# Optimization experiments

Hardware: AMD Instinct MI355X
Metric: run time of the kernel (lower is better)

## Reference

```python
import jax, jax.numpy as jnp
import numpy as np

IN_DIM = 512
OUT_DIM = 512
DEGREE = 3
KNOTS = (0.2, 0.4, 0.6, 0.8)
SDIM = DEGREE + 1 + len(KNOTS)  # 8
BATCH = 2048


def truncated_power_basis(t):
    # t: (B,) -> (B, SDIM)
    cols = [jnp.ones_like(t)]
    for p in range(1, DEGREE + 1):
        cols.append(t ** p)
    for c in KNOTS:  # degree > 1 branch: relu(t - knot)^degree
        cols.append(jax.nn.relu(t - c) ** DEGREE)
    return jnp.stack(cols, axis=1)


def setup_inputs() -> dict:
    key = jax.random.key(0)
    k0, k1, k2 = jax.random.split(key, 3)
    inputs = jax.random.uniform(k0, (BATCH, IN_DIM + 1), dtype=jnp.float32)
    # xavier_uniform for W_wts (fan_in=SDIM, fan_out=IN_DIM*OUT_DIM)
    limW = float(np.sqrt(6.0 / (SDIM + IN_DIM * OUT_DIM)))
    W_wts = jax.random.uniform(k1, (SDIM, IN_DIM * OUT_DIM), dtype=jnp.float32,
                               minval=-limW, maxval=limW)
    limb = float(np.sqrt(6.0 / (SDIM + OUT_DIM)))
    b_wts = jax.random.uniform(k2, (SDIM, OUT_DIM), dtype=jnp.float32,
                               minval=-limb, maxval=limb)
    return {"inputs": inputs, "W_wts": W_wts, "b_wts": b_wts}


def reference(inputs, W_wts, b_wts):
    treatment = inputs[:, 0]          # (B,)
    features = inputs[:, 1:]          # (B, IN_DIM)
    basis = truncated_power_basis(treatment)  # (B, SDIM)
    Wk = W_wts.reshape(SDIM, IN_DIM, OUT_DIM)
    # fused: per-sample weight W[b] = sum_s basis[b,s] * Wk[s]; out[b] = features[b] @ W[b]
    out = jnp.einsum('bs,bi,sio->bo', basis, features, Wk)
    out = out + basis @ b_wts         # (B, OUT_DIM)
    return out
```

## Files before the change

kernel.cpp:

```cpp
#include <hip/hip_runtime.h>
#include <stdint.h>

#define BATCH   2048
#define INDIM   512
#define OUTDIM  512
#define KP      4352
#define NBLK_A  2048
#define NBLK_B  544
#define SPLITK  4
#define KSTEPS  17

typedef __attribute__((ext_vector_type(4))) float  f32x4;
typedef __attribute__((ext_vector_type(8))) __bf16 bf16x8;
typedef __attribute__((ext_vector_type(8))) unsigned short u16x8;
typedef __attribute__((ext_vector_type(4))) unsigned short u16x4;

__device__ __forceinline__ unsigned short f2bf(float x) {
  unsigned int u = __float_as_uint(x);
  u += 0x7fffu + ((u >> 16) & 1u);
  return (unsigned short)(u >> 16);
}

__device__ __forceinline__ void llds16(const void* g, void* s) {
  __builtin_amdgcn_global_load_lds(
      (__attribute__((address_space(1))) void*)g,
      (__attribute__((address_space(3))) void*)s, 16, 0, 0);
}

__global__ __launch_bounds__(256) void prep_kernel(
    const float* __restrict__ inp, const float* __restrict__ W,
    const float* __restrict__ bwts, unsigned short* __restrict__ Abf,
    unsigned short* __restrict__ Btf) {
  const int tid = threadIdx.x;
  const int bx  = blockIdx.x;
  if (bx < NBLK_A) {
    const float* row = inp + (size_t)bx * (INDIM + 1);
    const float t = row[0];
    float bs[8];
    bs[0] = 1.0f; bs[1] = t; bs[2] = t * t; bs[3] = bs[2] * t;
    const float kn[4] = {0.2f, 0.4f, 0.6f, 0.8f};
#pragma unroll
    for (int c = 0; c < 4; ++c) {
      float d = fmaxf(t - kn[c], 0.0f);
      bs[4 + c] = d * d * d;
    }
    unsigned short* Arow = Abf + (size_t)bx * KP;
    for (int k4 = tid * 4; k4 < KP; k4 += 1024) {
      float v0, v1, v2, v3;
      if (k4 < 4096) {
        const float s = bs[k4 >> 9];
        const int i = k4 & 511;
        v0 = s * row[1 + i]; v1 = s * row[2 + i];
        v2 = s * row[3 + i]; v3 = s * row[4 + i];
      } else if (k4 < 4104) {
        const int s0 = k4 - 4096;
        v0 = bs[s0]; v1 = bs[s0 + 1]; v2 = bs[s0 + 2]; v3 = bs[s0 + 3];
      } else {
        v0 = v1 = v2 = v3 = 0.0f;
      }
      u16x4 o;
      o.x = f2bf(v0); o.y = f2bf(v1); o.z = f2bf(v2); o.w = f2bf(v3);
      *(u16x4*)&Arow[k4] = o;
    }
  } else {
    const int bb = bx - NBLK_A;
    const int kt = bb >> 3, ntile = bb & 7;
    const int k0 = kt * 64, n0 = ntile * 64;
    __shared__ float Ts[64][65];
#pragma unroll
    for (int p = 0; p < 4; ++p) {
      const int r  = (tid >> 4) + p * 16;
      const int c4 = (tid & 15) * 4;
      const int k  = k0 + r;
      float4 v;
      if (k < 4096)      v = *(const float4*)&W[(size_t)k * 512 + n0 + c4];
      else if (k < 4104) v = *(const float4*)&bwts[(size_t)(k - 4096) * 512 + n0 + c4];
      else               v = make_float4(0.f, 0.f, 0.f, 0.f);
      Ts[c4 + 0][r] = v.x; Ts[c4 + 1][r] = v.y;
      Ts[c4 + 2][r] = v.z; Ts[c4 + 3][r] = v.w;
    }
    __syncthreads();
    const int nl  = tid >> 2;
    const int kcc = (tid & 3) * 16;
    u16x8 o0, o1;
#pragma unroll
    for (int q = 0; q < 8; ++q) {
      o0[q] = f2bf(Ts[nl][kcc + q]);
      o1[q] = f2bf(Ts[nl][kcc + 8 + q]);
    }
    unsigned short* dst = Btf + (size_t)(n0 + nl) * KP + k0 + kcc;
    *(u16x8*)dst = o0;
    *(u16x8*)(dst + 8) = o1;
  }
}

__global__ __launch_bounds__(256, 4) void gemm_kernel(
    const unsigned short* __restrict__ Abf,
    const unsigned short* __restrict__ Btf,
    float* __restrict__ out) {
  const int tid  = threadIdx.x;
  const int kc   = blockIdx.x & (SPLITK - 1);
  const int tile = blockIdx.x >> 2;
  const int nt = tile & 7, mt = tile >> 3;
  const int m0 = mt * 64, n0 = nt * 64;
  const int l = tid & 63, w = tid >> 6;
  const int wm = w >> 1, wn = w & 1;
  const int quad = l >> 4, lr = l & 15;

  __shared__ __align__(16) unsigned short As[64 * 64];
  __shared__ __align__(16) unsigned short Bs[64 * 64];

  f32x4 acc00 = {}, acc01 = {}, acc10 = {}, acc11 = {};

  const int sr = tid >> 3, pc = tid & 7;
  const int lc = pc ^ (sr & 7);
  const unsigned short* Ag = Abf + (size_t)(m0 + sr) * KP + lc * 8;
  const unsigned short* Bg = Btf + (size_t)(n0 + sr) * KP + lc * 8;
  unsigned short* AsW = &As[sr * 64 + pc * 8];
  unsigned short* BsW = &Bs[sr * 64 + pc * 8];

  const int sx  = lr & 7;
  const int ar  = (wm * 32 + lr) * 64;
  const int br  = (wn * 32 + lr) * 64;
  const int c0  = ((0 + quad) ^ sx) * 8;
  const int c1  = ((4 + quad) ^ sx) * 8;

  int koff = kc * (KSTEPS * 64);
  for (int it = 0; it < KSTEPS; ++it) {
    llds16(Ag + koff,           AsW);
    llds16(Ag + koff + 32 * KP, AsW + 32 * 64);
    llds16(Bg + koff,           BsW);
    llds16(Bg + koff + 32 * KP, BsW + 32 * 64);
    __syncthreads();

    bf16x8 a00 = *(const bf16x8*)&As[ar + c0];
    bf16x8 a10 = *(const bf16x8*)&As[ar + 1024 + c0];
    bf16x8 b00 = *(const bf16x8*)&Bs[br + c0];
    bf16x8 b10 = *(const bf16x8*)&Bs[br + 1024 + c0];
    bf16x8 a01 = *(const bf16x8*)&As[ar + c1];
    bf16x8 a11 = *(const bf16x8*)&As[ar + 1024 + c1];
    bf16x8 b01 = *(const bf16x8*)&Bs[br + c1];
    bf16x8 b11 = *(const bf16x8*)&Bs[br + 1024 + c1];

    acc00 = __builtin_amdgcn_mfma_f32_16x16x32_bf16(a00, b00, acc00, 0, 0, 0);
    acc01 = __builtin_amdgcn_mfma_f32_16x16x32_bf16(a00, b10, acc01, 0, 0, 0);
    acc10 = __builtin_amdgcn_mfma_f32_16x16x32_bf16(a10, b00, acc10, 0, 0, 0);
    acc11 = __builtin_amdgcn_mfma_f32_16x16x32_bf16(a10, b10, acc11, 0, 0, 0);
    acc00 = __builtin_amdgcn_mfma_f32_16x16x32_bf16(a01, b01, acc00, 0, 0, 0);
    acc01 = __builtin_amdgcn_mfma_f32_16x16x32_bf16(a01, b11, acc01, 0, 0, 0);
    acc10 = __builtin_amdgcn_mfma_f32_16x16x32_bf16(a11, b01, acc10, 0, 0, 0);
    acc11 = __builtin_amdgcn_mfma_f32_16x16x32_bf16(a11, b11, acc11, 0, 0, 0);

    __syncthreads();
    koff += 64;
  }

  const int col = n0 + wn * 32 + lr;
  const int row = m0 + wm * 32 + quad * 4;
  float* o00 = out + (size_t)row * OUTDIM + col;
#pragma unroll
  for (int r = 0; r < 4; ++r) {
    unsafeAtomicAdd(o00 + (size_t)r * OUTDIM,             acc00[r]);
    unsafeAtomicAdd(o00 + (size_t)r * OUTDIM + 16,        acc01[r]);
    unsafeAtomicAdd(o00 + (size_t)(16 + r) * OUTDIM,      acc10[r]);
    unsafeAtomicAdd(o00 + (size_t)(16 + r) * OUTDIM + 16, acc11[r]);
  }
}

extern "C" void kernel_launch(void* const* d_in, const int* in_sizes, int n_in,
                              void* d_out, int out_size, void* d_ws, size_t ws_size,
                              hipStream_t stream) {
  const float* inp  = (const float*)d_in[0];
  const float* W    = (const float*)d_in[1];
  const float* bwts = (const float*)d_in[2];
  float* out = (float*)d_out;

  unsigned short* Abf = (unsigned short*)d_ws;
  unsigned short* Btf = Abf + (size_t)BATCH * KP;

  hipMemsetAsync(d_out, 0, (size_t)BATCH * OUTDIM * sizeof(float), stream);
  prep_kernel<<<NBLK_A + NBLK_B, 256, 0, stream>>>(inp, W, bwts, Abf, Btf);
  gemm_kernel<<<(BATCH / 64) * (OUTDIM / 64) * SPLITK, 256, 0, stream>>>(Abf, Btf, out);
}
```

Measured before the change: 101.9 us.

## Factor basis scaling out of GEMM: per-slice feature GEMM then scale by basis

The 2048x4352 basis-scaled activation matrix is no longer materialised. The GEMM now loads the bf16 features (2048x512) directly, computes a partial product for each basis slice, and scales it in fp32 by that row's basis value. The bias term basis@b_wts is computed in the prep kernel and written straight to the output, which removes the memset. This cuts prep-kernel write traffic and lets the A tile come from a much smaller, cache-resident array, at the cost of some extra fp32 FMAs per slice.

```diff
diff --git a/kernel.cpp b/kernel.cpp
--- a/kernel.cpp
+++ b/kernel.cpp
@@ -4,16 +4,13 @@
 #define BATCH   2048
 #define INDIM   512
 #define OUTDIM  512
-#define KP      4352
-#define NBLK_A  2048
-#define NBLK_B  544
+#define SDIM    8
+#define KTOT    4096
 #define SPLITK  4
-#define KSTEPS  17
 
 typedef __attribute__((ext_vector_type(4))) float  f32x4;
 typedef __attribute__((ext_vector_type(8))) __bf16 bf16x8;
 typedef __attribute__((ext_vector_type(8))) unsigned short u16x8;
-typedef __attribute__((ext_vector_type(4))) unsigned short u16x4;
 
 __device__ __forceinline__ unsigned short f2bf(float x) {
   unsigned int u = __float_as_uint(x);
@@ -27,55 +24,32 @@
       (__attribute__((address_space(3))) void*)s, 16, 0, 0);
 }
 
+__device__ __forceinline__ void mkbasis(float t, float* bs) {
+  bs[0] = 1.0f; bs[1] = t; bs[2] = t * t; bs[3] = bs[2] * t;
+  const float kn[4] = {0.2f, 0.4f, 0.6f, 0.8f};
+#pragma unroll
+  for (int c = 0; c < 4; ++c) {
+    float d = fmaxf(t - kn[c], 0.0f);
+    bs[4 + c] = d * d * d;
+  }
+}
+
 __global__ __launch_bounds__(256) void prep_kernel(
     const float* __restrict__ inp, const float* __restrict__ W,
-    const float* __restrict__ bwts, unsigned short* __restrict__ Abf,
-    unsigned short* __restrict__ Btf) {
+    const float* __restrict__ bwts, unsigned short* __restrict__ Fbf,
+    unsigned short* __restrict__ Btf, float* __restrict__ Bas,
+    float* __restrict__ out) {
   const int tid = threadIdx.x;
   const int bx  = blockIdx.x;
-  if (bx < NBLK_A) {
-    const float* row = inp + (size_t)bx * (INDIM + 1);
-    const float t = row[0];
-    float bs[8];
-    bs[0] = 1.0f; bs[1] = t; bs[2] = t * t; bs[3] = bs[2] * t;
-    const float kn[4] = {0.2f, 0.4f, 0.6f, 0.8f};
-#pragma unroll
-    for (int c = 0; c < 4; ++c) {
-      float d = fmaxf(t - kn[c], 0.0f);
-      bs[4 + c] = d * d * d;
-    }
-    unsigned short* Arow = Abf + (size_t)bx * KP;
-    for (int k4 = tid * 4; k4 < KP; k4 += 1024) {
-      float v0, v1, v2, v3;
-      if (k4 < 4096) {
-        const float s = bs[k4 >> 9];
-        const int i = k4 & 511;
-        v0 = s * row[1 + i]; v1 = s * row[2 + i];
-        v2 = s * row[3 + i]; v3 = s * row[4 + i];
-      } else if (k4 < 4104) {
-        const int s0 = k4 - 4096;
-        v0 = bs[s0]; v1 = bs[s0 + 1]; v2 = bs[s0 + 2]; v3 = bs[s0 + 3];
-      } else {
-        v0 = v1 = v2 = v3 = 0.0f;
-      }
-      u16x4 o;
-      o.x = f2bf(v0); o.y = f2bf(v1); o.z = f2bf(v2); o.w = f2bf(v3);
-      *(u16x4*)&Arow[k4] = o;
-    }
-  } else {
-    const int bb = bx - NBLK_A;
-    const int kt = bb >> 3, ntile = bb & 7;
+  if (bx < 512) {
+    const int kt = bx >> 3, ntile = bx & 7;
     const int k0 = kt * 64, n0 = ntile * 64;
     __shared__ float Ts[64][65];
 #pragma unroll
     for (int p = 0; p < 4; ++p) {
       const int r  = (tid >> 4) + p * 16;
       const int c4 = (tid & 15) * 4;
-      const int k  = k0 + r;
-      float4 v;
-      if (k < 4096)      v = *(const float4*)&W[(size_t)k * 512 + n0 + c4];
-      else if (k < 4104) v = *(const float4*)&bwts[(size_t)(k - 4096) * 512 + n0 + c4];
-      else               v = make_float4(0.f, 0.f, 0.f, 0.f);
+      float4 v = *(const float4*)&W[(size_t)(k0 + r) * 512 + n0 + c4];
       Ts[c4 + 0][r] = v.x; Ts[c4 + 1][r] = v.y;
       Ts[c4 + 2][r] = v.z; Ts[c4 + 3][r] = v.w;
     }
@@ -88,15 +62,47 @@
       o0[q] = f2bf(Ts[nl][kcc + q]);
       o1[q] = f2bf(Ts[nl][kcc + 8 + q]);
     }
-    unsigned short* dst = Btf + (size_t)(n0 + nl) * KP + k0 + kcc;
+    unsigned short* dst = Btf + (size_t)(n0 + nl) * KTOT + k0 + kcc;
     *(u16x8*)dst = o0;
     *(u16x8*)(dst + 8) = o1;
+  } else if (bx < 1024) {
+    const int b0   = (bx - 512) * 4;
+    const int b    = b0 + (tid >> 6);
+    const int i0   = (tid & 63) * 8;
+    const float* row = inp + (size_t)b * (INDIM + 1);
+    u16x8 o;
+#pragma unroll
+    for (int q = 0; q < 8; ++q) o[q] = f2bf(row[1 + i0 + q]);
+    *(u16x8*)(Fbf + (size_t)b * INDIM + i0) = o;
+    if (tid < 4) {
+      const int bb = b0 + tid;
+      float t = inp[(size_t)bb * (INDIM + 1)];
+      float bs[8]; mkbasis(t, bs);
+      f32x4 lo = {bs[0], bs[1], bs[2], bs[3]};
+      f32x4 hi = {bs[4], bs[5], bs[6], bs[7]};
+      *(f32x4*)(Bas + (size_t)bb * 8)     = lo;
+      *(f32x4*)(Bas + (size_t)bb * 8 + 4) = hi;
+    }
+  } else {
+    const int bb = (bx - 1024) * 2 + (tid >> 7);
+    const int o0 = (tid & 127) * 4;
+    float t = inp[(size_t)bb * (INDIM + 1)];
+    float bs[8]; mkbasis(t, bs);
+    float4 a = make_float4(0.f, 0.f, 0.f, 0.f);
+#pragma unroll
+    for (int s = 0; s < 8; ++s) {
+      float4 wv = *(const float4*)&bwts[s * OUTDIM + o0];
+      a.x += bs[s] * wv.x; a.y += bs[s] * wv.y;
+      a.z += bs[s] * wv.z; a.w += bs[s] * wv.w;
+    }
+    *(float4*)&out[(size_t)bb * OUTDIM + o0] = a;
   }
 }
 
 __global__ __launch_bounds__(256, 4) void gemm_kernel(
-    const unsigned short* __restrict__ Abf,
+    const unsigned short* __restrict__ Fbf,
     const unsigned short* __restrict__ Btf,
+    const float* __restrict__ Bas,
     float* __restrict__ out) {
   const int tid  = threadIdx.x;
   const int kc   = blockIdx.x & (SPLITK - 1);
@@ -110,12 +116,12 @@
   __shared__ __align__(16) unsigned short As[64 * 64];
   __shared__ __align__(16) unsigned short Bs[64 * 64];
 
-  f32x4 acc00 = {}, acc01 = {}, acc10 = {}, acc11 = {};
+  f32x4 m00 = {}, m01 = {}, m10 = {}, m11 = {};
 
   const int sr = tid >> 3, pc = tid & 7;
   const int lc = pc ^ (sr & 7);
-  const unsigned short* Ag = Abf + (size_t)(m0 + sr) * KP + lc * 8;
-  const unsigned short* Bg = Btf + (size_t)(n0 + sr) * KP + lc * 8;
+  const unsigned short* Ag = Fbf + (size_t)(m0 + sr) * INDIM + lc * 8;
+  const unsigned short* Bg = Btf + (size_t)(n0 + sr) * KTOT + lc * 8;
   unsigned short* AsW = &As[sr * 64 + pc * 8];
   unsigned short* BsW = &Bs[sr * 64 + pc * 8];
 
@@ -125,34 +131,48 @@
   const int c0  = ((0 + quad) ^ sx) * 8;
   const int c1  = ((4 + quad) ^ sx) * 8;
 
-  int koff = kc * (KSTEPS * 64);
-  for (int it = 0; it < KSTEPS; ++it) {
-    llds16(Ag + koff,           AsW);
-    llds16(Ag + koff + 32 * KP, AsW + 32 * 64);
-    llds16(Bg + koff,           BsW);
-    llds16(Bg + koff + 32 * KP, BsW + 32 * 64);
-    __syncthreads();
-
-    bf16x8 a00 = *(const bf16x8*)&As[ar + c0];
-    bf16x8 a10 = *(const bf16x8*)&As[ar + 1024 + c0];
-    bf16x8 b00 = *(const bf16x8*)&Bs[br + c0];
-    bf16x8 b10 = *(const bf16x8*)&Bs[br + 1024 + c0];
-    bf16x8 a01 = *(const bf16x8*)&As[ar + c1];
-    bf16x8 a11 = *(const bf16x8*)&As[ar + 1024 + c1];
-    bf16x8 b01 = *(const bf16x8*)&Bs[br + c1];
-    bf16x8 b11 = *(const bf16x8*)&Bs[br + 1024 + c1];
-
-    acc00 = __builtin_amdgcn_mfma_f32_16x16x32_bf16(a00, b00, acc00, 0, 0, 0);
-    acc01 = __builtin_amdgcn_mfma_f32_16x16x32_bf16(a00, b10, acc01, 0, 0, 0);
-    acc10 = __builtin_amdgcn_mfma_f32_16x16x32_bf16(a10, b00, acc10, 0, 0, 0);
-    acc11 = __builtin_amdgcn_mfma_f32_16x16x32_bf16(a10, b10, acc11, 0, 0, 0);
-    acc00 = __builtin_amdgcn_mfma_f32_16x16x32_bf16(a01, b01, acc00, 0, 0, 0);
-    acc01 = __builtin_amdgcn_mfma_f32_16x16x32_bf16(a01, b11, acc01, 0, 0, 0);
-    acc10 = __builtin_amdgcn_mfma_f32_16x16x32_bf16(a11, b01, acc10, 0, 0, 0);
-    acc11 = __builtin_amdgcn_mfma_f32_16x16x32_bf16(a11, b11, acc11, 0, 0, 0);
-
-    __syncthreads();
-    koff += 64;
+  const float* bp = Bas + (size_t)(m0 + wm * 32 + quad * 4) * 8;
+
+#pragma unroll
+  for (int sl = 0; sl < 2; ++sl) {
+    const int s = kc * 2 + sl;
+    const unsigned short* Bk = Bg + (size_t)s * 512;
+    f32x4 p00 = {}, p01 = {}, p10 = {}, p11 = {};
+    for (int ib = 0; ib < 8; ++ib) {
+      const int ka = ib * 64;
+      llds16(Ag + ka,               AsW);
+      llds16(Ag + ka + 32 * INDIM,  AsW + 32 * 64);
+      llds16(Bk + ka,               BsW);
+      llds16(Bk + ka + 32 * KTOT,   BsW + 32 * 64);
+      __syncthreads();
+
+      bf16x8 a00 = *(const bf16x8*)&As[ar + c0];
+      bf16x8 a10 = *(const bf16x8*)&As[ar + 1024 + c0];
+      bf16x8 b00 = *(const bf16x8*)&Bs[br + c0];
+      bf16x8 b10 = *(const bf16x8*)&Bs[br + 1024 + c0];
+      bf16x8 a01 = *(const bf16x8*)&As[ar + c1];
+      bf16x8 a11 = *(const bf16x8*)&As[ar + 1024 + c1];
+      bf16x8 b01 = *(const bf16x8*)&Bs[br + c1];
+      bf16x8 b11 = *(const bf16x8*)&Bs[br + 1024 + c1];
+
+      p00 = __builtin_amdgcn_mfma_f32_16x16x32_bf16(a00, b00, p00, 0, 0, 0);
+      p01 = __builtin_amdgcn_mfma_f32_16x16x32_bf16(a00, b10, p01, 0, 0, 0);
+      p10 = __builtin_amdgcn_mfma_f32_16x16x32_bf16(a10, b00, p10, 0, 0, 0);
+      p11 = __builtin_amdgcn_mfma_f32_16x16x32_bf16(a10, b10, p11, 0, 0, 0);
+      p00 = __builtin_amdgcn_mfma_f32_16x16x32_bf16(a01, b01, p00, 0, 0, 0);
+      p01 = __builtin_amdgcn_mfma_f32_16x16x32_bf16(a01, b11, p01, 0, 0, 0);
+      p10 = __builtin_amdgcn_mfma_f32_16x16x32_bf16(a11, b01, p10, 0, 0, 0);
+      p11 = __builtin_amdgcn_mfma_f32_16x16x32_bf16(a11, b11, p11, 0, 0, 0);
+
+      __syncthreads();
+    }
+#pragma unroll
+    for (int r = 0; r < 4; ++r) {
+      const float f0 = bp[r * 8 + s];
+      const float f1 = bp[(16 + r) * 8 + s];
+      m00[r] += p00[r] * f0; m01[r] += p01[r] * f0;
+      m10[r] += p10[r] * f1; m11[r] += p11[r] * f1;
+    }
   }
 
   const int col = n0 + wn * 32 + lr;
@@ -160,10 +180,10 @@
   float* o00 = out + (size_t)row * OUTDIM + col;
 #pragma unroll
   for (int r = 0; r < 4; ++r) {
-    unsafeAtomicAdd(o00 + (size_t)r * OUTDIM,             acc00[r]);
-    unsafeAtomicAdd(o00 + (size_t)r * OUTDIM + 16,        acc01[r]);
-    unsafeAtomicAdd(o00 + (size_t)(16 + r) * OUTDIM,      acc10[r]);
-    unsafeAtomicAdd(o00 + (size_t)(16 + r) * OUTDIM + 16, acc11[r]);
+    unsafeAtomicAdd(o00 + (size_t)r * OUTDIM,             m00[r]);
+    unsafeAtomicAdd(o00 + (size_t)r * OUTDIM + 16,        m01[r]);
+    unsafeAtomicAdd(o00 + (size_t)(16 + r) * OUTDIM,      m10[r]);
+    unsafeAtomicAdd(o00 + (size_t)(16 + r) * OUTDIM + 16, m11[r]);
   }
 }
 
@@ -175,10 +195,10 @@
   const float* bwts = (const float*)d_in[2];
   float* out = (float*)d_out;
 
-  unsigned short* Abf = (unsigned short*)d_ws;
-  unsigned short* Btf = Abf + (size_t)BATCH * KP;
-
-  hipMemsetAsync(d_out, 0, (size_t)BATCH * OUTDIM * sizeof(float), stream);
-  prep_kernel<<<NBLK_A + NBLK_B, 256, 0, stream>>>(inp, W, bwts, Abf, Btf);
-  gemm_kernel<<<(BATCH / 64) * (OUTDIM / 64) * SPLITK, 256, 0, stream>>>(Abf, Btf, out);
-}
+  unsigned short* Fbf = (unsigned short*)d_ws;
+  unsigned short* Btf = Fbf + (size_t)BATCH * INDIM;
+  float*          Bas = (float*)(Btf + (size_t)OUTDIM * KTOT);
+
+  prep_kernel<<<2048, 256, 0, stream>>>(inp, W, bwts, Fbf, Btf, Bas, out);
+  gemm_kernel<<<(BATCH / 64) * (OUTDIM / 64) * SPLITK, 256, 0, stream>>>(Fbf, Btf, Bas, out);
+}
```

Measured after the change: 92.96 us. 8.8% less time.
